# Optimization experiments

Measured on AMD Instinct MI355X. Metric: run time of the kernel, lower is better.

Reference implementation:

```python
import jax, jax.numpy as jnp
import numpy as np

N = 10000      # atoms
F = 32         # nr_atom_basis
H = 7          # nr_heads
C = F * H      # nr_coefficients = 224
E = 200000     # edges
NRBF = 50
CUTOFF = 5.0
EPS = 1e-8


def _seg_sum(x, idx, n):
    return jax.ops.segment_sum(x, idx, num_segments=n)


def _seg_mean(x, idx, n):
    # torch scatter_reduce 'mean' with include_self=False: sum/count, 0 for empty segments
    s = _seg_sum(x, idx, n)
    cnt = _seg_sum(jnp.ones((x.shape[0],), x.dtype), idx, n)
    cnt = jnp.maximum(cnt, 1.0).reshape((n,) + (1,) * (x.ndim - 1))
    return s / cnt


def _scatter_softmax(w, idx, n):
    m = jax.ops.segment_max(w, idx, num_segments=n)
    m = jnp.where(jnp.isfinite(m), m, 0.0)  # guard empty segments
    e = jnp.exp(w - m[idx])
    s = _seg_sum(e, idx, n)
    return e / s[idx]


def setup_inputs():
    key = jax.random.key(0)
    ks = jax.random.split(key, 16)
    def w(k, shape, scale=0.1):
        return jax.random.normal(k, shape, jnp.float32) * scale
    return {
        "h": w(ks[0], (N, F), 1.0),
        "x": w(ks[1], (N, 3), 1.0),
        "v": w(ks[2], (N, 3), 0.1),
        "pairlist": jax.random.randint(ks[3], (2, E), 0, N),
        "w_in": w(ks[4], (2 * F, NRBF)), "b_in": jnp.zeros((NRBF,), jnp.float32),
        "w_e1": w(ks[5], (2 * F + NRBF + 1, F)), "b_e1": jnp.zeros((F,), jnp.float32),
        "w_e2": w(ks[6], (F, F)), "b_e2": jnp.zeros((F,), jnp.float32),
        "w_att": w(ks[7], (F, H)), "b_att": jnp.zeros((H,), jnp.float32),
        "w_n1": w(ks[8], (F + C + F, F)), "b_n1": jnp.zeros((F,), jnp.float32),
        "w_n2": w(ks[9], (F, F)), "b_n2": jnp.zeros((F,), jnp.float32),
        "w_pn1": w(ks[10], (C, F)), "b_pn1": jnp.zeros((F,), jnp.float32),
        "w_pn2": w(ks[11], (F, F)), "b_pn2": jnp.zeros((F,), jnp.float32),
        "w_v1": w(ks[12], (F, F)), "b_v1": jnp.zeros((F,), jnp.float32),
        "w_v2": w(ks[13], (F, 1)),
        "w_xmix": w(ks[14], (C, C)),
        "w_vmix": w(ks[15], (C, 1)),
    }


def reference(h, x, v, pairlist, w_in, b_in, w_e1, b_e1, w_e2, b_e2,
              w_att, b_att, w_n1, b_n1, w_n2, b_n2, w_pn1, b_pn1,
              w_pn2, b_pn2, w_v1, b_v1, w_v2, w_xmix, w_vmix):
    act = jax.nn.silu
    idx_i, idx_j = pairlist[0], pairlist[1]
    n = h.shape[0]

    r_ij = x[idx_j] - x[idx_i]                      # [E,3]
    d_ij = jnp.linalg.norm(r_ij, axis=-1)           # [E]
    dir_ij = r_ij / (d_ij[:, None] + EPS)           # [E,3]

    # edge model: continuous-filter conv with concatenation
    h_cat = jnp.concatenate([h[idx_i], h[idx_j]], axis=-1)           # [E,2F]
    centers = jnp.linspace(0.0, CUTOFF, NRBF)
    width = centers[1] - centers[0]
    rbf = jnp.exp(-0.5 * ((d_ij[:, None] - centers) / width) ** 2)   # [E,NRBF]
    filt = rbf * (h_cat @ w_in + b_in)                               # [E,NRBF]
    edge_in = jnp.concatenate([h_cat, filt, d_ij[:, None]], axis=-1)
    h_ij_edge = act(edge_in @ w_e1 + b_e1) @ w_e2 + b_e2             # [E,F]

    # semantic attention (scatter softmax over edges grouped by idx_i)
    att_w = jax.nn.celu(h_ij_edge @ w_att + b_att, alpha=2.0)        # [E,H]
    cut = 0.5 * (jnp.cos(jnp.pi * d_ij / CUTOFF) + 1.0) * (d_ij < CUTOFF)
    att = _scatter_softmax(att_w * cut[:, None], idx_i, n)           # [E,H]
    # einsum('pf,ph->pfh').reshape -> f-major, h-minor
    h_ij_sem = (h_ij_edge[:, :, None] * att[:, None, :]).reshape(-1, C)  # [E,C]
    h_i_sem = _seg_sum(h_ij_sem, idx_i, n)                           # [N,C]

    # equivariant combinations + spatial attention
    comb = jnp.tanh(h_ij_sem @ w_xmix)[:, :, None] * dir_ij[:, None, :]  # [E,C,3]
    comb_mean = _seg_mean(comb, idx_i, n)                            # [N,C,3]
    cnsq = jnp.sum(comb_mean ** 2, axis=-1)                          # [N,C]
    h_i_spatial = act(act(cnsq @ w_pn1 + b_pn1) @ w_pn2 + b_pn2)     # [N,F]

    # node update
    node_in = jnp.concatenate([h, h_i_sem, h_i_spatial], axis=-1)
    h_upd = h + act(act(node_in @ w_n1 + b_n1) @ w_n2 + b_n2)        # [N,F]

    # velocity update
    v_ij = jnp.einsum('ecx,c->ex', comb, w_vmix[:, 0])               # [E,3]
    dv = _seg_mean(v_ij, idx_i, n)                                   # [N,3]
    gate = 2.0 * jax.nn.sigmoid(act(h @ w_v1 + b_v1) @ w_v2)         # [N,1]
    v_upd = gate * v + dv
    x_upd = x + v_upd
    return h_upd, x_upd, v_upd
```

## Files before the change

### kernel.cpp

```cpp
#include <hip/hip_runtime.h>
#include <hip/hip_bf16.h>
#include <math.h>

typedef unsigned short u16;
typedef __attribute__((ext_vector_type(8))) short bf16x8;
typedef __attribute__((ext_vector_type(4))) float f32x4;

constexpr int kF    = 32;
constexpr int kH    = 7;
constexpr int kC    = 224;
constexpr int kRBF  = 50;
constexpr int kM    = 128;
constexpr int kStr  = 232;
constexpr int kEM   = 128;
constexpr int kAStr = 136;
constexpr int kBStr = 40;
constexpr float kCut = 5.0f;
constexpr float kEps = 1e-8f;

__device__ __forceinline__ float silu_f(float a) { return a / (1.f + __expf(-a)); }
__device__ __forceinline__ float tanh_f(float x) {
    float e = __expf(2.f * x);
    return 1.f - 2.f / (e + 1.f);
}
__device__ __forceinline__ float bf2f(u16 u) {
    union { unsigned int i; float f; } v; v.i = ((unsigned int)u) << 16; return v.f;
}
__device__ __forceinline__ u16 f2bf(float f) {
    union { float f; unsigned int i; } v; v.f = f;
    unsigned int x = v.i;
    unsigned int round = ((x >> 16) & 1u) + 0x7fffu;
    return (u16)((x + round) >> 16);
}
__device__ __forceinline__ unsigned pk2(float a, float b) {
    union { __hip_bfloat162 h; unsigned u; } v;
    v.h = __float22bfloat162_rn(make_float2(a, b));
    return v.u;
}

__global__ __launch_bounds__(256) void init_kernel(
    const float* __restrict__ wx, const float* __restrict__ w_in,
    const float* __restrict__ w_e1, const float* __restrict__ w_e2,
    const float* __restrict__ w_att, const float* __restrict__ b_e2,
    const float* __restrict__ b_att, const int* __restrict__ pl,
    u16* __restrict__ wxT, u16* __restrict__ W1T, u16* __restrict__ W2T,
    u16* __restrict__ W3T, u16* __restrict__ W24T, float* __restrict__ b24,
    int* __restrict__ counts, int E_)
{
    int idx = blockIdx.x * 256 + threadIdx.x;
    if (idx < kC * kC) {
        int c = idx / kC, k = idx - c * kC;
        wxT[idx] = f2bf(wx[k * kC + c]);
    }
    for (int e = idx; e < E_; e += gridDim.x * 256) atomicAdd(&counts[pl[e]], 1);

    if (blockIdx.x == 0) {
        int t = threadIdx.x;
        for (int i = t; i < 64 * 64; i += 256) {
            int n = i >> 6, k = i & 63;
            W1T[i] = f2bf((n < kRBF) ? w_in[k * kRBF + n] : 0.f);
        }
        for (int i = t; i < 32 * 128; i += 256) {
            int n = i >> 7, k = i & 127;
            W2T[i] = f2bf((k < 115) ? w_e1[k * kF + n] : 0.f);
        }
        for (int i = t; i < 32 * 32; i += 256) {
            int n = i >> 5, k = i & 31;
            W3T[i] = f2bf(w_e2[k * kF + n]);
        }
        for (int i = t; i < 16 * 32; i += 256) {
            int n = i >> 5, k = i & 31;
            float a = 0.f;
            if (n < kH) for (int o = 0; o < kF; o++) a += w_e2[k * kF + o] * w_att[o * kH + n];
            W24T[i] = f2bf(a);
        }
        if (t < kH) {
            float a = b_att[t];
            for (int o = 0; o < kF; o++) a += b_e2[o] * w_att[o * kH + t];
            b24[t] = a;
        }
    }
}

__global__ __launch_bounds__(1024) void scan_kernel(
    const int* __restrict__ counts, int* __restrict__ offsets, int n)
{
    __shared__ int buf[1024];
    int t = threadIdx.x;
    int chunk = (n + 1023) >> 10;
    int lo = t * chunk;
    int s = 0;
    for (int i = 0; i < chunk; i++) {
        int g = lo + i;
        if (g < n) s += counts[g];
    }
    buf[t] = s;
    __syncthreads();
    for (int off = 1; off < 1024; off <<= 1) {
        int v = (t >= off) ? buf[t - off] : 0;
        __syncthreads();
        buf[t] += v;
        __syncthreads();
    }
    int run = buf[t] - s;
    for (int i = 0; i < chunk; i++) {
        int g = lo + i;
        if (g < n) { offsets[g] = run; run += counts[g]; }
    }
    if (t == 1023) offsets[n] = buf[1023];
}

__global__ __launch_bounds__(256) void edge_kernel(
    const float* __restrict__ h, const float* __restrict__ x,
    const int* __restrict__ pl, const int* __restrict__ offs,
    int* __restrict__ cursor, int* __restrict__ nid, int E_,
    const float* __restrict__ b_in, const float* __restrict__ b_e1,
    const float* __restrict__ b_e2,
    const u16* __restrict__ W1T, const u16* __restrict__ W2T,
    const u16* __restrict__ W3T, const u16* __restrict__ W24T,
    const float* __restrict__ b24,
    u16* __restrict__ he_g, float* __restrict__ logit_g,
    float* __restrict__ dir_g)
{
    __shared__ __align__(16) u16 s_A[kEM][kAStr];
    __shared__ __align__(16) u16 s_t1[kEM][kBStr];
    __shared__ float s_d[kEM];
    __shared__ int   s_r[kEM];

    int t = threadIdx.x;
    int T0 = blockIdx.x * kEM;
    int w = t >> 6, lane = t & 63, quad = lane >> 4, l15 = lane & 15;

    {
        int e = t >> 1, half = t & 1;
        int ge = T0 + e;
        bool val = ge < E_;
        int i = 0, j = 0;
        if (val) { i = pl[ge]; j = pl[E_ + ge]; }
        const float4* pi = (const float4*)(h + (size_t)i * kF) + half * 4;
        const float4* pj = (const float4*)(h + (size_t)j * kF) + half * 4;
#pragma unroll
        for (int q = 0; q < 4; q++) {
            float4 a = val ? pi[q] : make_float4(0.f, 0.f, 0.f, 0.f);
            float4 b = val ? pj[q] : make_float4(0.f, 0.f, 0.f, 0.f);
            unsigned* di = (unsigned*)&s_A[e][half * 16 + 4 * q];
            di[0] = pk2(a.x, a.y); di[1] = pk2(a.z, a.w);
            unsigned* dj = (unsigned*)&s_A[e][kF + half * 16 + 4 * q];
            dj[0] = pk2(b.x, b.y); dj[1] = pk2(b.z, b.w);
        }
        if (half == 0) {
            float d = 0.f;
            int r = 0;
            if (val) {
                int p = atomicAdd(&cursor[i], 1);
                r = offs[i] + p;
                nid[r] = i;
                float r0 = x[j * 3 + 0] - x[i * 3 + 0];
                float r1 = x[j * 3 + 1] - x[i * 3 + 1];
                float r2 = x[j * 3 + 2] - x[i * 3 + 2];
                d = sqrtf(r0 * r0 + r1 * r1 + r2 * r2);
                float inv = 1.0f / (d + kEps);
                dir_g[(size_t)r * 3 + 0] = r0 * inv;
                dir_g[(size_t)r * 3 + 1] = r1 * inv;
                dir_g[(size_t)r * 3 + 2] = r2 * inv;
            }
            s_r[e] = r;
            s_d[e] = d;
            s_A[e][114] = f2bf(d);
            s_A[e][115] = 0;
            unsigned* z = (unsigned*)&s_A[e][116];
#pragma unroll
            for (int q = 0; q < 6; q++) z[q] = 0u;
        }
    }
    __syncthreads();

    const float invw = 49.0f / kCut;

    {
        bf16x8 a1[2][2];
#pragma unroll
        for (int rt = 0; rt < 2; rt++)
#pragma unroll
            for (int kt = 0; kt < 2; kt++)
                a1[rt][kt] = *(const bf16x8*)&s_A[32 * w + 16 * rt + l15][kt * 32 + quad * 8];
#pragma unroll
        for (int ct = 0; ct < 4; ct++) {
            int c = ct * 16 + l15;
            bf16x8 b0 = *(const bf16x8*)(W1T + (size_t)c * 64 + quad * 8);
            bf16x8 b1 = *(const bf16x8*)(W1T + (size_t)c * 64 + 32 + quad * 8);
            float bin = (c < kRBF) ? b_in[c] : 0.f;
#pragma unroll
            for (int rt = 0; rt < 2; rt++) {
                f32x4 acc = {0.f, 0.f, 0.f, 0.f};
                acc = __builtin_amdgcn_mfma_f32_16x16x32_bf16(a1[rt][0], b0, acc, 0, 0, 0);
                acc = __builtin_amdgcn_mfma_f32_16x16x32_bf16(a1[rt][1], b1, acc, 0, 0, 0);
                if (c < kRBF) {
#pragma unroll
                    for (int r = 0; r < 4; r++) {
                        int row = 32 * w + 16 * rt + quad * 4 + r;
                        float arg = s_d[row] * invw - (float)c;
                        float filt = __expf(-0.5f * arg * arg) * (acc[r] + bin);
                        s_A[row][64 + c] = f2bf(filt);
                    }
                }
            }
        }
    }

    {
        bf16x8 a2[2][4];
#pragma unroll
        for (int rt = 0; rt < 2; rt++)
#pragma unroll
            for (int kt = 0; kt < 4; kt++)
                a2[rt][kt] = *(const bf16x8*)&s_A[32 * w + 16 * rt + l15][kt * 32 + quad * 8];
#pragma unroll
        for (int ct = 0; ct < 2; ct++) {
            int c = ct * 16 + l15;
            bf16x8 bb[4];
#pragma unroll
            for (int kt = 0; kt < 4; kt++)
                bb[kt] = *(const bf16x8*)(W2T + (size_t)c * 128 + kt * 32 + quad * 8);
            float be = b_e1[c];
#pragma unroll
            for (int rt = 0; rt < 2; rt++) {
                f32x4 acc = {0.f, 0.f, 0.f, 0.f};
#pragma unroll
                for (int kt = 0; kt < 4; kt++)
                    acc = __builtin_amdgcn_mfma_f32_16x16x32_bf16(a2[rt][kt], bb[kt], acc, 0, 0, 0);
#pragma unroll
                for (int r = 0; r < 4; r++) {
                    int row = 32 * w + 16 * rt + quad * 4 + r;
                    s_t1[row][c] = f2bf(silu_f(acc[r] + be));
                }
            }
        }
    }

    {
        bf16x8 a3[2];
#pragma unroll
        for (int rt = 0; rt < 2; rt++)
            a3[rt] = *(const bf16x8*)&s_t1[32 * w + 16 * rt + l15][quad * 8];

#pragma unroll
        for (int ct = 0; ct < 2; ct++) {
            int c = ct * 16 + l15;
            bf16x8 b3 = *(const bf16x8*)(W3T + (size_t)c * 32 + quad * 8);
            float be = b_e2[c];
#pragma unroll
            for (int rt = 0; rt < 2; rt++) {
                f32x4 acc = {0.f, 0.f, 0.f, 0.f};
                acc = __builtin_amdgcn_mfma_f32_16x16x32_bf16(a3[rt], b3, acc, 0, 0, 0);
#pragma unroll
                for (int r = 0; r < 4; r++) {
                    int row = 32 * w + 16 * rt + quad * 4 + r;
                    int ge = T0 + row;
                    if (ge < E_) he_g[(size_t)s_r[row] * kF + c] = f2bf(acc[r] + be);
                }
            }
        }
        {
            bf16x8 b4 = *(const bf16x8*)(W24T + (size_t)l15 * 32 + quad * 8);
            float bb = (l15 < kH) ? b24[l15] : 0.f;
#pragma unroll
            for (int rt = 0; rt < 2; rt++) {
                f32x4 acc = {0.f, 0.f, 0.f, 0.f};
                acc = __builtin_amdgcn_mfma_f32_16x16x32_bf16(a3[rt], b4, acc, 0, 0, 0);
                if (l15 < kH) {
#pragma unroll
                    for (int r = 0; r < 4; r++) {
                        int row = 32 * w + 16 * rt + quad * 4 + r;
                        int ge = T0 + row;
                        if (ge < E_) {
                            float a = acc[r] + bb;
                            a = (a >= 0.f) ? a : 2.f * (__expf(0.5f * a) - 1.f);
                            float dd = s_d[row];
                            float cut = (dd < kCut)
                                ? 0.5f * (__cosf(0.62831853071795864f * dd) + 1.f) : 0.f;
                            logit_g[(size_t)s_r[row] * kH + l15] = a * cut;
                        }
                    }
                }
            }
        }
    }
}

__global__ __launch_bounds__(256) void stats_kernel(
    const float* __restrict__ logit_g, const int* __restrict__ offsets,
    float* __restrict__ m_g, float* __restrict__ invs_g, int N_)
{
    int grp  = threadIdx.x >> 5;
    int lane = threadIdx.x & 31;
    int node = blockIdx.x * 8 + grp;
    if (node >= N_) return;
    int base = offsets[node];
    int deg  = offsets[node + 1] - base;

    float m[kH], ss[kH];
#pragma unroll
    for (int hh = 0; hh < kH; hh++) { m[hh] = -1e30f; ss[hh] = 0.f; }
    for (int e = lane; e < deg; e += 32) {
        const float* lp = logit_g + (size_t)(base + e) * kH;
#pragma unroll
        for (int hh = 0; hh < kH; hh++) {
            float vv = lp[hh];
            if (vv > m[hh]) { ss[hh] *= __expf(m[hh] - vv); m[hh] = vv; }
            ss[hh] += __expf(vv - m[hh]);
        }
    }
#pragma unroll
    for (int hh = 0; hh < kH; hh++) {
        float mm = m[hh], s2 = ss[hh];
#pragma unroll
        for (int off = 16; off >= 1; off >>= 1) {
            float mo = __shfl_xor(mm, off);
            float so = __shfl_xor(s2, off);
            float mn = fmaxf(mm, mo);
            s2 = s2 * __expf(mm - mn) + so * __expf(mo - mn);
            mm = mn;
        }
        if (lane == 0) {
            m_g[(size_t)node * kH + hh] = mm;
            invs_g[(size_t)node * kH + hh] = (s2 > 0.f) ? 1.f / s2 : 0.f;
        }
    }
}

__global__ __launch_bounds__(256) void xmix_kernel(
    const u16* __restrict__ he_g, const float* __restrict__ logit_g,
    const float* __restrict__ dir_g, const int* __restrict__ nid,
    const float* __restrict__ m_g, const float* __restrict__ invs_g,
    const u16* __restrict__ wxT, int E_,
    float* __restrict__ nodeacc, float* __restrict__ bpart, int* __restrict__ bid)
{
    __shared__ __align__(16) u16 s_buf[kM][kStr];
    __shared__ float s_att[kM][kH];
    __shared__ __align__(16) float s_dir4[kM][4];
    __shared__ int   s_node[kM];
    __shared__ int   s_prev, s_next;

    int t = threadIdx.x;
    int T0 = blockIdx.x * kM;
    int cp = min(kM, E_ - T0);

    if (t < kM) s_node[t] = (T0 + t < E_) ? nid[T0 + t] : -1;
    if (t == 0) {
        s_prev = (T0 > 0) ? nid[T0 - 1] : -2;
        s_next = (T0 + cp < E_) ? nid[T0 + cp] : -2;
    }
    __syncthreads();

    int w    = t >> 6;
    int lane = t & 63;
    int quad = lane >> 4;
    int l15  = lane & 15;

    int ws = 32 * w;
    int we = min(ws + 32, cp);
    bool winvalid = (ws < cp);
    bool contL = false, contR = false;
    if (winvalid) {
        int nfirst = s_node[ws], nlast = s_node[we - 1];
        contL = (w == 0) ? (s_prev == nfirst) : (s_node[ws - 1] == nfirst);
        contR = (we == cp) ? (s_next == nlast) : (s_node[we] == nlast);
    }
    if (lane == 0) {
        int b0 = -1, b1 = -1;
        if (winvalid) {
            int nfirst = s_node[ws], nlast = s_node[we - 1];
            b0 = contL ? nfirst : -1;
            if (contR && !(nfirst == nlast && contL)) b1 = nlast;
        }
        bid[8 * blockIdx.x + 2 * w + 0] = b0;
        bid[8 * blockIdx.x + 2 * w + 1] = b1;
    }
    bool active_w = winvalid && (lane < 56);
    int c0 = 4 * lane;

    for (int idx = t; idx < kM * kH; idx += 256) {
        int e = idx / kH, hh = idx - e * kH;
        float a = 0.f;
        if (T0 + e < E_) {
            int nd = s_node[e];
            a = __expf(logit_g[(size_t)(T0 + e) * kH + hh] - m_g[(size_t)nd * kH + hh])
                * invs_g[(size_t)nd * kH + hh];
        }
        s_att[e][hh] = a;
    }
    for (int idx = t; idx < cp * 3; idx += 256) {
        int e = idx / 3, xx = idx - e * 3;
        s_dir4[e][xx] = dir_g[(size_t)(T0 + e) * 3 + xx];
    }
    __syncthreads();

#pragma unroll
    for (int p = 0; p < kM * kF / 256; p++) {
        int idx = t + 256 * p;
        int e = idx >> 5, f = idx & 31;
        float hv = (T0 + e < E_) ? bf2f(he_g[(size_t)(T0 + e) * kF + f]) : 0.f;
        float sv[7];
#pragma unroll
        for (int hh = 0; hh < kH; hh++) sv[hh] = hv * s_att[e][hh];
        u16* dst = &s_buf[e][f * 7];
        if ((f & 1) == 0) {
            *(unsigned*)(dst)     = pk2(sv[0], sv[1]);
            *(unsigned*)(dst + 2) = pk2(sv[2], sv[3]);
            *(unsigned*)(dst + 4) = pk2(sv[4], sv[5]);
            dst[6] = f2bf(sv[6]);
        } else {
            dst[0] = f2bf(sv[0]);
            *(unsigned*)(dst + 1) = pk2(sv[1], sv[2]);
            *(unsigned*)(dst + 3) = pk2(sv[3], sv[4]);
            *(unsigned*)(dst + 5) = pk2(sv[5], sv[6]);
        }
    }
    __syncthreads();

    if (active_w) {
        float hs0 = 0.f, hs1 = 0.f, hs2 = 0.f, hs3 = 0.f;
        int rs = ws;
        for (int e = ws; e < we; e++) {
            if (s_node[e] != s_node[rs]) {
                bool comp = (rs > ws) || !contL;
                float4 vv = make_float4(hs0, hs1, hs2, hs3);
                if (comp) *(float4*)&nodeacc[(size_t)s_node[rs] * 896 + 672 + c0] = vv;
                else *(float4*)&bpart[(size_t)(8 * blockIdx.x + 2 * w) * 896 + 672 + c0] = vv;
                hs0 = hs1 = hs2 = hs3 = 0.f; rs = e;
            }
            uint2 pv = *(const uint2*)&s_buf[e][c0];
            hs0 += bf2f((u16)pv.x); hs1 += bf2f((u16)(pv.x >> 16));
            hs2 += bf2f((u16)pv.y); hs3 += bf2f((u16)(pv.y >> 16));
        }
        bool t0 = (rs == ws);
        bool comp = ((!t0) || !contL) && !contR;
        float4 vv = make_float4(hs0, hs1, hs2, hs3);
        if (comp) *(float4*)&nodeacc[(size_t)s_node[rs] * 896 + 672 + c0] = vv;
        else {
            int slot = (t0 && contL) ? 0 : 1;
            *(float4*)&bpart[(size_t)(8 * blockIdx.x + 2 * w + slot) * 896 + 672 + c0] = vv;
        }
    }

    bf16x8 afr[2][7];
#pragma unroll
    for (int rt = 0; rt < 2; rt++)
#pragma unroll
        for (int kt = 0; kt < 7; kt++)
            afr[rt][kt] = *(const bf16x8*)&s_buf[32 * w + 16 * rt + l15][kt * 32 + quad * 8];

    bf16x8 bb[4][7];
#pragma unroll
    for (int b = 0; b < 3; b++)
#pragma unroll
        for (int kt = 0; kt < 7; kt++)
            bb[b][kt] = *(const bf16x8*)(wxT + (size_t)(16 * b + l15) * kC + kt * 32 + quad * 8);
    __syncthreads();

#pragma unroll
    for (int ct = 0; ct < 14; ct++) {
        const int cur = ct & 3;
        const int nxt = (ct + 3) & 3;
        if (ct < 11) {
            const u16* bp = wxT + (size_t)((ct + 3) * 16 + l15) * kC + quad * 8;
#pragma unroll
            for (int kt = 0; kt < 7; kt++) bb[nxt][kt] = *(const bf16x8*)(bp + kt * 32);
        }
        f32x4 acc0 = {0.f, 0.f, 0.f, 0.f};
        f32x4 acc1 = {0.f, 0.f, 0.f, 0.f};
#pragma unroll
        for (int kt = 0; kt < 7; kt++) {
            acc0 = __builtin_amdgcn_mfma_f32_16x16x32_bf16(afr[0][kt], bb[cur][kt], acc0, 0, 0, 0);
            acc1 = __builtin_amdgcn_mfma_f32_16x16x32_bf16(afr[1][kt], bb[cur][kt], acc1, 0, 0, 0);
        }
        int colg = ct * 16 + l15;
#pragma unroll
        for (int s = 0; s < 2; s++) {
            f32x4 ac = s ? acc1 : acc0;
            int rbase = 32 * w + 16 * s + quad * 4;
            unsigned p01 = pk2(tanh_f(ac[0]), tanh_f(ac[1]));
            unsigned p23 = pk2(tanh_f(ac[2]), tanh_f(ac[3]));
            s_buf[rbase + 0][colg] = (u16)p01;
            s_buf[rbase + 1][colg] = (u16)(p01 >> 16);
            s_buf[rbase + 2][colg] = (u16)p23;
            s_buf[rbase + 3][colg] = (u16)(p23 >> 16);
        }
    }
    __syncthreads();

    if (active_w) {
        float a0[4] = {0.f, 0.f, 0.f, 0.f};
        float a1[4] = {0.f, 0.f, 0.f, 0.f};
        float a2[4] = {0.f, 0.f, 0.f, 0.f};
        int rs = ws;
        for (int e = ws; e < we; e++) {
            if (s_node[e] != s_node[rs]) {
                bool comp = (rs > ws) || !contL;
                float* p = comp ? (nodeacc + (size_t)s_node[rs] * 896)
                                : (bpart + (size_t)(8 * blockIdx.x + 2 * w) * 896);
                *(float4*)&p[c0]       = make_float4(a0[0], a0[1], a0[2], a0[3]);
                *(float4*)&p[224 + c0] = make_float4(a1[0], a1[1], a1[2], a1[3]);
                *(float4*)&p[448 + c0] = make_float4(a2[0], a2[1], a2[2], a2[3]);
#pragma unroll
                for (int q = 0; q < 4; q++) { a0[q] = 0.f; a1[q] = 0.f; a2[q] = 0.f; }
                rs = e;
            }
            float4 dd = *(const float4*)&s_dir4[e][0];
            uint2 pv = *(const uint2*)&s_buf[e][c0];
            float Tv[4];
            Tv[0] = bf2f((u16)pv.x); Tv[1] = bf2f((u16)(pv.x >> 16));
            Tv[2] = bf2f((u16)pv.y); Tv[3] = bf2f((u16)(pv.y >> 16));
#pragma unroll
            for (int q = 0; q < 4; q++) {
                a0[q] += Tv[q] * dd.x;
                a1[q] += Tv[q] * dd.y;
                a2[q] += Tv[q] * dd.z;
            }
        }
        bool t0 = (rs == ws);
        bool comp = ((!t0) || !contL) && !contR;
        float* p;
        if (comp) p = nodeacc + (size_t)s_node[rs] * 896;
        else {
            int slot = (t0 && contL) ? 0 : 1;
            p = bpart + (size_t)(8 * blockIdx.x + 2 * w + slot) * 896;
        }
        *(float4*)&p[c0]       = make_float4(a0[0], a0[1], a0[2], a0[3]);
        *(float4*)&p[224 + c0] = make_float4(a1[0], a1[1], a1[2], a1[3]);
        *(float4*)&p[448 + c0] = make_float4(a2[0], a2[1], a2[2], a2[3]);
    }
}

__global__ __launch_bounds__(256) void node_kernel(
    const float* __restrict__ h, const float* __restrict__ x, const float* __restrict__ v,
    const float* __restrict__ nodeacc, const float* __restrict__ bpart,
    const int* __restrict__ bid, const int* __restrict__ offs,
    const float* __restrict__ w_n1, const float* __restrict__ b_n1,
    const float* __restrict__ w_n2, const float* __restrict__ b_n2,
    const float* __restrict__ w_pn1, const float* __restrict__ b_pn1,
    const float* __restrict__ w_pn2, const float* __restrict__ b_pn2,
    const float* __restrict__ w_v1, const float* __restrict__ b_v1,
    const float* __restrict__ w_v2, const float* __restrict__ w_vmix,
    float* __restrict__ out_h, float* __restrict__ out_x, float* __restrict__ out_v,
    int N_)
{
    __shared__ float s_cm[4][3][kC];
    __shared__ float s_cnsq[4][kC];
    __shared__ float s_ni[4][288];
    __shared__ float s_part[8][4][kF];
    __shared__ float s_hn[4][kF], s_sp1[4][kF], s_spat[4][kF], s_n1v[4][kF], s_g1[4][kF];
    __shared__ float s_pdv[4][3][8];
    __shared__ float s_gate[4], s_dv[4][3];

    int t = threadIdx.x;
    int n0 = blockIdx.x * 4;

    if (t < kC) {
        for (int nd = 0; nd < 4; nd++) {
            int node = n0 + nd;
            if (node >= N_) break;
            int base = offs[node], end = offs[node + 1];
            int deg = end - base;
            float a0 = 0.f, a1 = 0.f, a2 = 0.f, hh = 0.f;
            if (deg > 0) {
                int wlo = base >> 5, whi = (end - 1) >> 5;
                if (wlo == whi) {
                    const float* p = nodeacc + (size_t)node * 896;
                    a0 = p[t]; a1 = p[224 + t]; a2 = p[448 + t]; hh = p[672 + t];
                } else {
                    for (int W = wlo; W <= whi; W++) {
#pragma unroll
                        for (int s = 0; s < 2; s++) {
                            if (bid[2 * W + s] == node) {
                                const float* p = bpart + (size_t)(2 * W + s) * 896;
                                a0 += p[t]; a1 += p[224 + t]; a2 += p[448 + t]; hh += p[672 + t];
                            }
                        }
                    }
                }
            }
            float invc = 1.f / fmaxf((float)deg, 1.f);
            float m0 = a0 * invc, m1 = a1 * invc, m2 = a2 * invc;
            s_cm[nd][0][t] = m0; s_cm[nd][1][t] = m1; s_cm[nd][2][t] = m2;
            s_cnsq[nd][t] = m0 * m0 + m1 * m1 + m2 * m2;
            s_ni[nd][kF + t] = hh;
        }
    } else {
        int ln = t - 224;
        for (int nd = 0; nd < 4; nd++) {
            int node = n0 + nd;
            float hv = (node < N_) ? h[(size_t)node * kF + ln] : 0.f;
            s_hn[nd][ln] = hv;
            s_ni[nd][ln] = hv;
        }
    }
    __syncthreads();

    int o = t & 31, g = t >> 5;
    {
        float acc[4] = {0.f, 0.f, 0.f, 0.f};
        int cb = g * 28;
        for (int i = 0; i < 28; i++) {
            float wv = w_pn1[(cb + i) * kF + o];
#pragma unroll
            for (int nd = 0; nd < 4; nd++) acc[nd] += s_cnsq[nd][cb + i] * wv;
        }
#pragma unroll
        for (int nd = 0; nd < 4; nd++) s_part[g][nd][o] = acc[nd];
    }
    __syncthreads();
    if (t < 128) {
        int nd = t >> 5;
        float a = b_pn1[o];
#pragma unroll
        for (int g2 = 0; g2 < 8; g2++) a += s_part[g2][nd][o];
        s_sp1[nd][o] = silu_f(a);
    } else {
        int nd = (t - 128) >> 5;
        float a = b_v1[o];
        for (int f = 0; f < kF; f++) a += s_hn[nd][f] * w_v1[f * kF + o];
        s_g1[nd][o] = silu_f(a);
    }
    __syncthreads();
    if (t < 128) {
        int nd = t >> 5;
        float a = b_pn2[o];
        for (int o2 = 0; o2 < kF; o2++) a += s_sp1[nd][o2] * w_pn2[o2 * kF + o];
        s_spat[nd][o] = silu_f(a);
    } else if (t < 132) {
        int nd = t - 128;
        float a = 0.f;
        for (int o2 = 0; o2 < kF; o2++) a += s_g1[nd][o2] * w_v2[o2];
        s_gate[nd] = 2.f / (1.f + __expf(-a));
    } else if (t >= 160) {
        int q = t - 160; int nd = q / 24; int r = q - nd * 24;
        int xx = r >> 3, ln = r & 7;
        float a = 0.f;
        for (int c = ln; c < kC; c += 8) a += w_vmix[c] * s_cm[nd][xx][c];
        s_pdv[nd][xx][ln] = a;
    }
    __syncthreads();
    if (t < 128) {
        int nd = t >> 5;
        s_ni[nd][kF + kC + o] = s_spat[nd][o];
    } else if (t < 140) {
        int q = t - 128; int nd = q / 3; int xx = q - nd * 3;
        float a = 0.f;
#pragma unroll
        for (int ln = 0; ln < 8; ln++) a += s_pdv[nd][xx][ln];
        s_dv[nd][xx] = a;
    }
    __syncthreads();
    {
        float acc[4] = {0.f, 0.f, 0.f, 0.f};
        int rb = g * 36;
        for (int i = 0; i < 36; i++) {
            float wv = w_n1[(rb + i) * kF + o];
#pragma unroll
            for (int nd = 0; nd < 4; nd++) acc[nd] += s_ni[nd][rb + i] * wv;
        }
#pragma unroll
        for (int nd = 0; nd < 4; nd++) s_part[g][nd][o] = acc[nd];
    }
    __syncthreads();
    if (t < 128) {
        int nd = t >> 5;
        float a = b_n1[o];
#pragma unroll
        for (int g2 = 0; g2 < 8; g2++) a += s_part[g2][nd][o];
        s_n1v[nd][o] = silu_f(a);
    }
    __syncthreads();
    if (t < 128) {
        int nd = t >> 5; int node = n0 + nd;
        if (node < N_) {
            float a = b_n2[o];
            for (int o2 = 0; o2 < kF; o2++) a += s_n1v[nd][o2] * w_n2[o2 * kF + o];
            out_h[(size_t)node * kF + o] = s_hn[nd][o] + silu_f(a);
        }
    } else if (t < 140) {
        int q = t - 128; int nd = q / 3; int xx = q - nd * 3;
        int node = n0 + nd;
        if (node < N_) {
            float vv = v[(size_t)node * 3 + xx];
            float vu = s_gate[nd] * vv + s_dv[nd][xx];
            out_v[(size_t)node * 3 + xx] = vu;
            out_x[(size_t)node * 3 + xx] = x[(size_t)node * 3 + xx] + vu;
        }
    }
}

extern "C" void kernel_launch(void* const* d_in, const int* in_sizes, int n_in,
                              void* d_out, int out_size, void* d_ws, size_t ws_size,
                              hipStream_t stream)
{
    const float* h      = (const float*)d_in[0];
    const float* x      = (const float*)d_in[1];
    const float* v      = (const float*)d_in[2];
    const int*   pl     = (const int*)d_in[3];
    const float* w_in   = (const float*)d_in[4];
    const float* b_in   = (const float*)d_in[5];
    const float* w_e1   = (const float*)d_in[6];
    const float* b_e1   = (const float*)d_in[7];
    const float* w_e2   = (const float*)d_in[8];
    const float* b_e2   = (const float*)d_in[9];
    const float* w_att  = (const float*)d_in[10];
    const float* b_att  = (const float*)d_in[11];
    const float* w_n1   = (const float*)d_in[12];
    const float* b_n1   = (const float*)d_in[13];
    const float* w_n2   = (const float*)d_in[14];
    const float* b_n2   = (const float*)d_in[15];
    const float* w_pn1  = (const float*)d_in[16];
    const float* b_pn1  = (const float*)d_in[17];
    const float* w_pn2  = (const float*)d_in[18];
    const float* b_pn2  = (const float*)d_in[19];
    const float* w_v1   = (const float*)d_in[20];
    const float* b_v1   = (const float*)d_in[21];
    const float* w_v2   = (const float*)d_in[22];
    const float* w_xmix = (const float*)d_in[23];
    const float* w_vmix = (const float*)d_in[24];

    const int E_ = in_sizes[3] / 2;
    const int N_ = in_sizes[0] / kF;
    const int nblk = (E_ + kM - 1) / kM;

    char* w = (char*)d_ws;
    u16*   wxT     = (u16*)w;   w += (size_t)kC * kC * 2;
    u16*   W1T     = (u16*)w;   w += (size_t)64 * 64 * 2;
    u16*   W2T     = (u16*)w;   w += (size_t)32 * 128 * 2;
    u16*   W3T     = (u16*)w;   w += (size_t)32 * 32 * 2;
    u16*   W24T    = (u16*)w;   w += (size_t)16 * 32 * 2;
    float* b24     = (float*)w; w += 8 * 4;
    u16*   he_g    = (u16*)w;   w += (size_t)E_ * kF * 2;
    float* logit_g = (float*)w; w += (size_t)E_ * kH * 4;
    float* dir_g   = (float*)w; w += (size_t)E_ * 3 * 4;
    float* m_g     = (float*)w; w += (size_t)N_ * kH * 4;
    float* invs_g  = (float*)w; w += (size_t)N_ * kH * 4;
    float* nodeacc = (float*)w; w += (size_t)N_ * 896 * 4;
    float* bpart   = (float*)w; w += (size_t)8 * nblk * 896 * 4;
    int*   bid     = (int*)w;   w += (size_t)8 * nblk * 4;
    int* counts    = (int*)w;   w += (size_t)N_ * 4;
    int* offs      = (int*)w;   w += (size_t)(N_ + 1) * 4;
    int* cursor    = (int*)w;   w += (size_t)N_ * 4;
    int* nid       = (int*)w;   w += (size_t)E_ * 4;

    float* out_h = (float*)d_out;
    float* out_x = out_h + (size_t)N_ * kF;
    float* out_v = out_x + (size_t)N_ * 3;

    hipMemsetAsync(counts, 0, (size_t)N_ * 4, stream);
    hipMemsetAsync(cursor, 0, (size_t)N_ * 4, stream);

    init_kernel<<<dim3((kC * kC + 255) / 256), dim3(256), 0, stream>>>(
        w_xmix, w_in, w_e1, w_e2, w_att, b_e2, b_att, pl,
        wxT, W1T, W2T, W3T, W24T, b24, counts, E_);

    scan_kernel<<<dim3(1), dim3(1024), 0, stream>>>(counts, offs, N_);

    edge_kernel<<<dim3((E_ + kEM - 1) / kEM), dim3(256), 0, stream>>>(
        h, x, pl, offs, cursor, nid, E_, b_in, b_e1, b_e2,
        W1T, W2T, W3T, W24T, b24, he_g, logit_g, dir_g);

    stats_kernel<<<dim3((N_ + 7) / 8), dim3(256), 0, stream>>>(
        logit_g, offs, m_g, invs_g, N_);

    xmix_kernel<<<dim3(nblk), dim3(256), 0, stream>>>(
        he_g, logit_g, dir_g, nid, m_g, invs_g, wxT, E_,
        nodeacc, bpart, bid);

    node_kernel<<<dim3((N_ + 3) / 4), dim3(256), 0, stream>>>(
        h, x, v, nodeacc, bpart, bid, offs,
        w_n1, b_n1, w_n2, b_n2, w_pn1, b_pn1, w_pn2, b_pn2,
        w_v1, b_v1, w_v2, w_vmix, out_h, out_x, out_v, N_);
}
```

Measured before the change: 334.7 us.

## Project semantic features through w_n1 per edge before segment sum

Uses linearity to multiply each edge's 224-wide semantic vector by the h_sem slice of w_n1 with MFMA inside the xmix kernel, then segment-sums only 32 values per node instead of 224. This removes the separate 224-column segmented reduction and shrinks the node-kernel n1 matvec from 288 inputs to 64. It also trims the B-fragment prefetch ring from four slots to three and drops one barrier to cut register pressure. The cost is extra MFMA work per edge and an additional bf16 rounding of the projected values.

```diff
diff --git a/kernel.cpp b/kernel.cpp
--- a/kernel.cpp
+++ b/kernel.cpp
@@ -12,6 +12,7 @@
 constexpr int kRBF  = 50;
 constexpr int kM    = 128;
 constexpr int kStr  = 232;
+constexpr int kUSt  = 36;
 constexpr int kEM   = 128;
 constexpr int kAStr = 136;
 constexpr int kBStr = 40;
@@ -42,10 +43,11 @@
     const float* __restrict__ wx, const float* __restrict__ w_in,
     const float* __restrict__ w_e1, const float* __restrict__ w_e2,
     const float* __restrict__ w_att, const float* __restrict__ b_e2,
-    const float* __restrict__ b_att, const int* __restrict__ pl,
+    const float* __restrict__ b_att, const float* __restrict__ w_n1,
+    const int* __restrict__ pl,
     u16* __restrict__ wxT, u16* __restrict__ W1T, u16* __restrict__ W2T,
-    u16* __restrict__ W3T, u16* __restrict__ W24T, float* __restrict__ b24,
-    int* __restrict__ counts, int E_)
+    u16* __restrict__ W3T, u16* __restrict__ W24T, u16* __restrict__ Wn1hT,
+    float* __restrict__ b24, int* __restrict__ counts, int E_)
 {
     int idx = blockIdx.x * 256 + threadIdx.x;
     if (idx < kC * kC) {
@@ -78,6 +80,13 @@
             float a = b_att[t];
             for (int o = 0; o < kF; o++) a += b_e2[o] * w_att[o * kH + t];
             b24[t] = a;
+        }
+    }
+    if (blockIdx.x == 1) {
+        int t = threadIdx.x;
+        for (int i = t; i < 32 * kC; i += 256) {
+            int o = i / kC, k = i - o * kC;
+            Wn1hT[i] = f2bf(w_n1[(kF + k) * kF + o]);
         }
     }
 }
@@ -333,10 +342,11 @@
     const u16* __restrict__ he_g, const float* __restrict__ logit_g,
     const float* __restrict__ dir_g, const int* __restrict__ nid,
     const float* __restrict__ m_g, const float* __restrict__ invs_g,
-    const u16* __restrict__ wxT, int E_,
+    const u16* __restrict__ wxT, const u16* __restrict__ Wn1hT, int E_,
     float* __restrict__ nodeacc, float* __restrict__ bpart, int* __restrict__ bid)
 {
     __shared__ __align__(16) u16 s_buf[kM][kStr];
+    __shared__ __align__(8)  u16 s_U[kM][kUSt];
     __shared__ float s_att[kM][kH];
     __shared__ __align__(16) float s_dir4[kM][4];
     __shared__ int   s_node[kM];
@@ -419,31 +429,6 @@
     }
     __syncthreads();
 
-    if (active_w) {
-        float hs0 = 0.f, hs1 = 0.f, hs2 = 0.f, hs3 = 0.f;
-        int rs = ws;
-        for (int e = ws; e < we; e++) {
-            if (s_node[e] != s_node[rs]) {
-                bool comp = (rs > ws) || !contL;
-                float4 vv = make_float4(hs0, hs1, hs2, hs3);
-                if (comp) *(float4*)&nodeacc[(size_t)s_node[rs] * 896 + 672 + c0] = vv;
-                else *(float4*)&bpart[(size_t)(8 * blockIdx.x + 2 * w) * 896 + 672 + c0] = vv;
-                hs0 = hs1 = hs2 = hs3 = 0.f; rs = e;
-            }
-            uint2 pv = *(const uint2*)&s_buf[e][c0];
-            hs0 += bf2f((u16)pv.x); hs1 += bf2f((u16)(pv.x >> 16));
-            hs2 += bf2f((u16)pv.y); hs3 += bf2f((u16)(pv.y >> 16));
-        }
-        bool t0 = (rs == ws);
-        bool comp = ((!t0) || !contL) && !contR;
-        float4 vv = make_float4(hs0, hs1, hs2, hs3);
-        if (comp) *(float4*)&nodeacc[(size_t)s_node[rs] * 896 + 672 + c0] = vv;
-        else {
-            int slot = (t0 && contL) ? 0 : 1;
-            *(float4*)&bpart[(size_t)(8 * blockIdx.x + 2 * w + slot) * 896 + 672 + c0] = vv;
-        }
-    }
-
     bf16x8 afr[2][7];
 #pragma unroll
     for (int rt = 0; rt < 2; rt++)
@@ -451,20 +436,20 @@
         for (int kt = 0; kt < 7; kt++)
             afr[rt][kt] = *(const bf16x8*)&s_buf[32 * w + 16 * rt + l15][kt * 32 + quad * 8];
 
-    bf16x8 bb[4][7];
-#pragma unroll
-    for (int b = 0; b < 3; b++)
-#pragma unroll
-        for (int kt = 0; kt < 7; kt++)
-            bb[b][kt] = *(const bf16x8*)(wxT + (size_t)(16 * b + l15) * kC + kt * 32 + quad * 8);
-    __syncthreads();
+    bf16x8 bb[3][7];
+#pragma unroll
+    for (int kt = 0; kt < 7; kt++)
+        bb[0][kt] = *(const bf16x8*)(wxT + (size_t)l15 * kC + kt * 32 + quad * 8);
+#pragma unroll
+    for (int kt = 0; kt < 7; kt++)
+        bb[1][kt] = *(const bf16x8*)(wxT + (size_t)(16 + l15) * kC + kt * 32 + quad * 8);
 
 #pragma unroll
     for (int ct = 0; ct < 14; ct++) {
-        const int cur = ct & 3;
-        const int nxt = (ct + 3) & 3;
-        if (ct < 11) {
-            const u16* bp = wxT + (size_t)((ct + 3) * 16 + l15) * kC + quad * 8;
+        const int cur = ct % 3;
+        const int nxt = (ct + 2) % 3;
+        if (ct < 12) {
+            const u16* bp = wxT + (size_t)((ct + 2) * 16 + l15) * kC + quad * 8;
 #pragma unroll
             for (int kt = 0; kt < 7; kt++) bb[nxt][kt] = *(const bf16x8*)(bp + kt * 32);
         }
@@ -488,12 +473,36 @@
             s_buf[rbase + 3][colg] = (u16)(p23 >> 16);
         }
     }
-    __syncthreads();
+
+#pragma unroll
+    for (int ut = 0; ut < 2; ut++) {
+        bf16x8 ub[7];
+        const u16* bp = Wn1hT + (size_t)(ut * 16 + l15) * kC + quad * 8;
+#pragma unroll
+        for (int kt = 0; kt < 7; kt++) ub[kt] = *(const bf16x8*)(bp + kt * 32);
+        f32x4 acc0 = {0.f, 0.f, 0.f, 0.f};
+        f32x4 acc1 = {0.f, 0.f, 0.f, 0.f};
+#pragma unroll
+        for (int kt = 0; kt < 7; kt++) {
+            acc0 = __builtin_amdgcn_mfma_f32_16x16x32_bf16(afr[0][kt], ub[kt], acc0, 0, 0, 0);
+            acc1 = __builtin_amdgcn_mfma_f32_16x16x32_bf16(afr[1][kt], ub[kt], acc1, 0, 0, 0);
+        }
+        int ucol = ut * 16 + l15;
+#pragma unroll
+        for (int s = 0; s < 2; s++) {
+            f32x4 ac = s ? acc1 : acc0;
+            int rbase = 32 * w + 16 * s + quad * 4;
+#pragma unroll
+            for (int r = 0; r < 4; r++) s_U[rbase + r][ucol] = f2bf(ac[r]);
+        }
+    }
 
     if (active_w) {
+        bool uact = (lane < 8);
         float a0[4] = {0.f, 0.f, 0.f, 0.f};
         float a1[4] = {0.f, 0.f, 0.f, 0.f};
         float a2[4] = {0.f, 0.f, 0.f, 0.f};
+        float uu[4] = {0.f, 0.f, 0.f, 0.f};
         int rs = ws;
         for (int e = ws; e < we; e++) {
             if (s_node[e] != s_node[rs]) {
@@ -503,8 +512,9 @@
                 *(float4*)&p[c0]       = make_float4(a0[0], a0[1], a0[2], a0[3]);
                 *(float4*)&p[224 + c0] = make_float4(a1[0], a1[1], a1[2], a1[3]);
                 *(float4*)&p[448 + c0] = make_float4(a2[0], a2[1], a2[2], a2[3]);
-#pragma unroll
-                for (int q = 0; q < 4; q++) { a0[q] = 0.f; a1[q] = 0.f; a2[q] = 0.f; }
+                if (uact) *(float4*)&p[672 + c0] = make_float4(uu[0], uu[1], uu[2], uu[3]);
+#pragma unroll
+                for (int q = 0; q < 4; q++) { a0[q] = 0.f; a1[q] = 0.f; a2[q] = 0.f; uu[q] = 0.f; }
                 rs = e;
             }
             float4 dd = *(const float4*)&s_dir4[e][0];
@@ -517,6 +527,11 @@
                 a0[q] += Tv[q] * dd.x;
                 a1[q] += Tv[q] * dd.y;
                 a2[q] += Tv[q] * dd.z;
+            }
+            if (uact) {
+                uint2 uv = *(const uint2*)&s_U[e][c0];
+                uu[0] += bf2f((u16)uv.x); uu[1] += bf2f((u16)(uv.x >> 16));
+                uu[2] += bf2f((u16)uv.y); uu[3] += bf2f((u16)(uv.y >> 16));
             }
         }
         bool t0 = (rs == ws);
@@ -530,6 +545,7 @@
         *(float4*)&p[c0]       = make_float4(a0[0], a0[1], a0[2], a0[3]);
         *(float4*)&p[224 + c0] = make_float4(a1[0], a1[1], a1[2], a1[3]);
         *(float4*)&p[448 + c0] = make_float4(a2[0], a2[1], a2[2], a2[3]);
+        if (uact) *(float4*)&p[672 + c0] = make_float4(uu[0], uu[1], uu[2], uu[3]);
     }
 }
 
@@ -548,7 +564,8 @@
 {
     __shared__ float s_cm[4][3][kC];
     __shared__ float s_cnsq[4][kC];
-    __shared__ float s_ni[4][288];
+    __shared__ float s_ni[4][64];
+    __shared__ float s_usum[4][kF];
     __shared__ float s_part[8][4][kF];
     __shared__ float s_hn[4][kF], s_sp1[4][kF], s_spat[4][kF], s_n1v[4][kF], s_g1[4][kF];
     __shared__ float s_pdv[4][3][8];
@@ -568,14 +585,16 @@
                 int wlo = base >> 5, whi = (end - 1) >> 5;
                 if (wlo == whi) {
                     const float* p = nodeacc + (size_t)node * 896;
-                    a0 = p[t]; a1 = p[224 + t]; a2 = p[448 + t]; hh = p[672 + t];
+                    a0 = p[t]; a1 = p[224 + t]; a2 = p[448 + t];
+                    if (t < kF) hh = p[672 + t];
                 } else {
                     for (int W = wlo; W <= whi; W++) {
 #pragma unroll
                         for (int s = 0; s < 2; s++) {
                             if (bid[2 * W + s] == node) {
                                 const float* p = bpart + (size_t)(2 * W + s) * 896;
-                                a0 += p[t]; a1 += p[224 + t]; a2 += p[448 + t]; hh += p[672 + t];
+                                a0 += p[t]; a1 += p[224 + t]; a2 += p[448 + t];
+                                if (t < kF) hh += p[672 + t];
                             }
                         }
                     }
@@ -585,7 +604,7 @@
             float m0 = a0 * invc, m1 = a1 * invc, m2 = a2 * invc;
             s_cm[nd][0][t] = m0; s_cm[nd][1][t] = m1; s_cm[nd][2][t] = m2;
             s_cnsq[nd][t] = m0 * m0 + m1 * m1 + m2 * m2;
-            s_ni[nd][kF + t] = hh;
+            if (t < kF) s_usum[nd][t] = hh;
         }
     } else {
         int ln = t - 224;
@@ -644,7 +663,7 @@
     __syncthreads();
     if (t < 128) {
         int nd = t >> 5;
-        s_ni[nd][kF + kC + o] = s_spat[nd][o];
+        s_ni[nd][kF + o] = s_spat[nd][o];
     } else if (t < 140) {
         int q = t - 128; int nd = q / 3; int xx = q - nd * 3;
         float a = 0.f;
@@ -655,11 +674,13 @@
     __syncthreads();
     {
         float acc[4] = {0.f, 0.f, 0.f, 0.f};
-        int rb = g * 36;
-        for (int i = 0; i < 36; i++) {
-            float wv = w_n1[(rb + i) * kF + o];
-#pragma unroll
-            for (int nd = 0; nd < 4; nd++) acc[nd] += s_ni[nd][rb + i] * wv;
+        int rb = g * 8;
+        for (int i = 0; i < 8; i++) {
+            int r = rb + i;
+            int wr = (r < kF) ? r : (r + kC);
+            float wv = w_n1[wr * kF + o];
+#pragma unroll
+            for (int nd = 0; nd < 4; nd++) acc[nd] += s_ni[nd][r] * wv;
         }
 #pragma unroll
         for (int nd = 0; nd < 4; nd++) s_part[g][nd][o] = acc[nd];
@@ -667,7 +688,7 @@
     __syncthreads();
     if (t < 128) {
         int nd = t >> 5;
-        float a = b_n1[o];
+        float a = b_n1[o] + s_usum[nd][o];
 #pragma unroll
         for (int g2 = 0; g2 < 8; g2++) a += s_part[g2][nd][o];
         s_n1v[nd][o] = silu_f(a);
@@ -732,6 +753,7 @@
     u16*   W2T     = (u16*)w;   w += (size_t)32 * 128 * 2;
     u16*   W3T     = (u16*)w;   w += (size_t)32 * 32 * 2;
     u16*   W24T    = (u16*)w;   w += (size_t)16 * 32 * 2;
+    u16*   Wn1hT   = (u16*)w;   w += (size_t)32 * kC * 2;
     float* b24     = (float*)w; w += 8 * 4;
     u16*   he_g    = (u16*)w;   w += (size_t)E_ * kF * 2;
     float* logit_g = (float*)w; w += (size_t)E_ * kH * 4;
@@ -754,8 +776,8 @@
     hipMemsetAsync(cursor, 0, (size_t)N_ * 4, stream);
 
     init_kernel<<<dim3((kC * kC + 255) / 256), dim3(256), 0, stream>>>(
-        w_xmix, w_in, w_e1, w_e2, w_att, b_e2, b_att, pl,
-        wxT, W1T, W2T, W3T, W24T, b24, counts, E_);
+        w_xmix, w_in, w_e1, w_e2, w_att, b_e2, b_att, w_n1, pl,
+        wxT, W1T, W2T, W3T, W24T, Wn1hT, b24, counts, E_);
 
     scan_kernel<<<dim3(1), dim3(1024), 0, stream>>>(counts, offs, N_);
 
@@ -767,7 +789,7 @@
         logit_g, offs, m_g, invs_g, N_);
 
     xmix_kernel<<<dim3(nblk), dim3(256), 0, stream>>>(
-        he_g, logit_g, dir_g, nid, m_g, invs_g, wxT, E_,
+        he_g, logit_g, dir_g, nid, m_g, invs_g, wxT, Wn1hT, E_,
         nodeacc, bpart, bid);
 
     node_kernel<<<dim3((N_ + 3) / 4), dim3(256), 0, stream>>>(
```

Measured after the change: 321.2 us. 4.0% less time.
